# Optimization experiments

Measured on AMD Instinct MI355X. Metric: run time of the kernel, lower is better.

Reference implementation:

```python
import jax, jax.numpy as jnp
import numpy as np

EMBED = 768
NH = 12          # num_heads
NL = 3           # num_levels
NP = 4           # num_points
DV = 384         # value dim = embed_dim * deform_ratio(0.5)
DH = DV // NH    # per-head value dim = 32
B = 16
LQ = 1024        # (512/16)^2 ViT tokens
SHAPES = [(64, 64), (32, 32), (16, 16)]  # 1/8, 1/16, 1/32 pyramid of 512x512
LKV = sum(h * w for h, w in SHAPES)      # 5376
EPS = 1e-6


def layer_norm(x, w, b):
    mu = jnp.mean(x, axis=-1, keepdims=True)
    var = jnp.mean((x - mu) ** 2, axis=-1, keepdims=True)
    return (x - mu) / jnp.sqrt(var + EPS) * w + b


def bilinear_sample(v, loc, H, W):
    # v: (B, NH, H*W, DH); loc: (B, Lq, NH, P, 2) normalized in [0,1]
    # Matches torch grid_sample(align_corners=False, padding_mode='zeros').
    Bv, Lq = loc.shape[0], loc.shape[1]
    x = loc[..., 0] * W - 0.5
    y = loc[..., 1] * H - 0.5
    x0 = jnp.floor(x)
    y0 = jnp.floor(y)
    dx = x - x0
    dy = y - y0
    x0i = x0.astype(jnp.int32)
    y0i = y0.astype(jnp.int32)

    def gather(xi, yi):
        valid = (xi >= 0) & (xi < W) & (yi >= 0) & (yi < H)  # (B,Lq,NH,P)
        xc = jnp.clip(xi, 0, W - 1)
        yc = jnp.clip(yi, 0, H - 1)
        lin = (yc * W + xc).transpose(0, 2, 1, 3).reshape(Bv, NH, Lq * NP)
        g = jnp.take_along_axis(v, lin[..., None], axis=2)  # (B,NH,Lq*P,DH)
        g = g.reshape(Bv, NH, Lq, NP, DH).transpose(0, 2, 1, 3, 4)  # (B,Lq,NH,P,DH)
        return g * valid[..., None].astype(g.dtype)

    g00 = gather(x0i, y0i)
    g01 = gather(x0i + 1, y0i)
    g10 = gather(x0i, y0i + 1)
    g11 = gather(x0i + 1, y0i + 1)
    w00 = ((1 - dx) * (1 - dy))[..., None]
    w01 = (dx * (1 - dy))[..., None]
    w10 = ((1 - dx) * dy)[..., None]
    w11 = (dx * dy)[..., None]
    return g00 * w00 + g01 * w01 + g10 * w10 + g11 * w11


def ms_deform_attn_core(value, shapes_list, loc, aw):
    # value: (B,LKV,NH,DH); loc: (B,Lq,NH,NL,NP,2); aw: (B,Lq,NH,NL,NP)
    Bv, Lq = loc.shape[0], loc.shape[1]
    samples = []
    idx = 0
    for l, (H, W) in enumerate(shapes_list):
        v = value[:, idx:idx + H * W].transpose(0, 2, 1, 3)  # (B,NH,HW,DH)
        idx += H * W
        samples.append(bilinear_sample(v, loc[:, :, :, l], H, W))
    s = jnp.stack(samples, axis=3)  # (B,Lq,NH,NL,NP,DH)
    o = jnp.einsum('bqhlp,bqhlpd->bqhd', aw, s)
    return o.reshape(Bv, Lq, NH * DH)


def setup_inputs() -> dict:
    key = jax.random.key(0)
    ks = jax.random.split(key, 12)

    def n(k, shape, s=0.02):
        return jax.random.normal(k, shape, jnp.float32) * s

    return {
        'q': jax.random.normal(ks[0], (B, LQ, EMBED), jnp.float32),
        'reference_points': jax.random.uniform(ks[1], (B, LQ, NL, 2), jnp.float32),
        'kv': jax.random.normal(ks[2], (B, LKV, EMBED), jnp.float32),
        'spatial_shapes': jnp.asarray(SHAPES, jnp.int32),
        'level_start_index': jnp.asarray(
            np.cumsum([0] + [h * w for h, w in SHAPES])[:-1], jnp.int32),
        'ln1_w': jnp.ones(EMBED, jnp.float32),
        'ln1_b': jnp.zeros(EMBED, jnp.float32),
        'ln2_w': jnp.ones(EMBED, jnp.float32),
        'ln2_b': jnp.zeros(EMBED, jnp.float32),
        'gamma': n(ks[3], (EMBED,), 0.1),
        'w_off': n(ks[4], (EMBED, NH * NL * NP * 2)),
        'b_off': n(ks[5], (NH * NL * NP * 2,), 0.01),
        'w_aw': n(ks[6], (EMBED, NH * NL * NP)),
        'b_aw': jnp.zeros(NH * NL * NP, jnp.float32),
        'w_val': n(ks[7], (EMBED, DV)),
        'b_val': jnp.zeros(DV, jnp.float32),
        'w_out': n(ks[8], (DV, EMBED)),
        'b_out': jnp.zeros(EMBED, jnp.float32),
    }


def reference(q, reference_points, kv, spatial_shapes, level_start_index,
              ln1_w, ln1_b, ln2_w, ln2_b, gamma,
              w_off, b_off, w_aw, b_aw, w_val, b_val, w_out, b_out):
    shapes_list = [tuple(int(v) for v in r) for r in np.asarray(spatial_shapes)]
    Bq, Lq, _ = q.shape
    qn = layer_norm(q, ln1_w, ln1_b)
    kvn = layer_norm(kv, ln2_w, ln2_b)
    value = (kvn @ w_val + b_val).reshape(Bq, -1, NH, DH)
    off = (qn @ w_off + b_off).reshape(Bq, Lq, NH, NL, NP, 2)
    aw = (qn @ w_aw + b_aw).reshape(Bq, Lq, NH, NL * NP)
    aw = jax.nn.softmax(aw, axis=-1).reshape(Bq, Lq, NH, NL, NP)
    # offset normalizer is (W_l, H_l) per level
    wh = jnp.asarray([[w, h] for (h, w) in shapes_list], q.dtype)  # (NL,2)
    loc = reference_points[:, :, None, :, None, :] + off / wh[None, None, None, :, None, :]
    attn = ms_deform_attn_core(value, shapes_list, loc, aw)
    attn = attn @ w_out + b_out
    return q + gamma * attn
```

## Files before the change

kernel.cpp:

```cpp
#include <hip/hip_runtime.h>

#define DEV __device__ __forceinline__

typedef short bf16x8 __attribute__((ext_vector_type(8)));
typedef float f32x4 __attribute__((ext_vector_type(4)));
typedef unsigned int u32;
typedef __attribute__((address_space(1))) const u32* gas_ptr;
typedef __attribute__((address_space(3))) u32* las_ptr;

DEV short f2bf(float f) {
  union { float f; unsigned u; } un; un.f = f;
  unsigned r = un.u + 0x7FFFu + ((un.u >> 16) & 1u);
  return (short)(r >> 16);
}
DEV float bf2f(unsigned short s) {
  union { unsigned u; float f; } un;
  un.u = ((unsigned)s) << 16;
  return un.f;
}
DEV void gload16(const short* g, short* l) {
  __builtin_amdgcn_global_load_lds((gas_ptr)g, (las_ptr)l, 16, 0, 0);
}
DEV float hsum4(float4 v) { return v.x + v.y + v.z + v.w; }

DEV void ln_row4(const float* __restrict__ x, const float* __restrict__ w,
                 const float* __restrict__ b, short* __restrict__ y,
                 const int rb) {
  const int wv = threadIdx.x >> 6, lane = threadIdx.x & 63;
  const int row = rb * 4 + wv;
  const float* xr = x + (size_t)row * 768;
  float4 v0 = *(const float4*)(xr + lane * 4);
  float4 v1 = *(const float4*)(xr + 256 + lane * 4);
  float4 v2 = *(const float4*)(xr + 512 + lane * 4);
  float s = hsum4(v0) + hsum4(v1) + hsum4(v2);
  #pragma unroll
  for (int off = 32; off > 0; off >>= 1) s += __shfl_xor(s, off, 64);
  const float mu = s * (1.f / 768.f);
  float4 d0 = make_float4(v0.x - mu, v0.y - mu, v0.z - mu, v0.w - mu);
  float4 d1 = make_float4(v1.x - mu, v1.y - mu, v1.z - mu, v1.w - mu);
  float4 d2 = make_float4(v2.x - mu, v2.y - mu, v2.z - mu, v2.w - mu);
  float vs = d0.x * d0.x + d0.y * d0.y + d0.z * d0.z + d0.w * d0.w +
             d1.x * d1.x + d1.y * d1.y + d1.z * d1.z + d1.w * d1.w +
             d2.x * d2.x + d2.y * d2.y + d2.z * d2.z + d2.w * d2.w;
  #pragma unroll
  for (int off = 32; off > 0; off >>= 1) vs += __shfl_xor(vs, off, 64);
  const float rs = rsqrtf(vs * (1.f / 768.f) + 1e-6f);
  const float4 w0 = *(const float4*)(w + lane * 4);
  const float4 w1 = *(const float4*)(w + 256 + lane * 4);
  const float4 w2 = *(const float4*)(w + 512 + lane * 4);
  const float4 b0 = *(const float4*)(b + lane * 4);
  const float4 b1 = *(const float4*)(b + 256 + lane * 4);
  const float4 b2 = *(const float4*)(b + 512 + lane * 4);
  unsigned short* yr = (unsigned short*)y + (size_t)row * 768;
  ushort4 o;
  o.x = (unsigned short)f2bf(d0.x * rs * w0.x + b0.x);
  o.y = (unsigned short)f2bf(d0.y * rs * w0.y + b0.y);
  o.z = (unsigned short)f2bf(d0.z * rs * w0.z + b0.z);
  o.w = (unsigned short)f2bf(d0.w * rs * w0.w + b0.w);
  *(ushort4*)(yr + lane * 4) = o;
  o.x = (unsigned short)f2bf(d1.x * rs * w1.x + b1.x);
  o.y = (unsigned short)f2bf(d1.y * rs * w1.y + b1.y);
  o.z = (unsigned short)f2bf(d1.z * rs * w1.z + b1.z);
  o.w = (unsigned short)f2bf(d1.w * rs * w1.w + b1.w);
  *(ushort4*)(yr + 256 + lane * 4) = o;
  o.x = (unsigned short)f2bf(d2.x * rs * w2.x + b2.x);
  o.y = (unsigned short)f2bf(d2.y * rs * w2.y + b2.y);
  o.z = (unsigned short)f2bf(d2.z * rs * w2.z + b2.z);
  o.w = (unsigned short)f2bf(d2.w * rs * w2.w + b2.w);
  *(ushort4*)(yr + 512 + lane * 4) = o;
}

__global__ __launch_bounds__(256) void fused_pre_kernel(
    const float* __restrict__ kv, const float* __restrict__ q,
    const float* __restrict__ ln2w, const float* __restrict__ ln2b,
    const float* __restrict__ ln1w, const float* __restrict__ ln1b,
    short* __restrict__ kvn, short* __restrict__ qn,
    const float* __restrict__ w_val, const float* __restrict__ w_off,
    const float* __restrict__ w_aw, const float* __restrict__ w_out,
    const float* __restrict__ b_off, const float* __restrict__ b_aw,
    short* __restrict__ wT_val, short* __restrict__ wT_offaw,
    short* __restrict__ wT_out, float* __restrict__ bias_cat) {
  const int bid = blockIdx.x;
  if (bid < 21504) { ln_row4(kv, ln2w, ln2b, kvn, bid); return; }
  if (bid < 25600) { ln_row4(q, ln1w, ln1b, qn, bid - 21504); return; }
  int g = (bid - 25600) * 256 + threadIdx.x;
  bf16x8 v;
  if (g < 36864) {
    int n = g / 96, k0 = (g % 96) * 8;
    #pragma unroll
    for (int i = 0; i < 8; i++) v[i] = f2bf(w_val[(size_t)(k0 + i) * 384 + n]);
    *(bf16x8*)&wT_val[n * 768 + k0] = v;
    return;
  }
  g -= 36864;
  if (g < 27648) {
    int n = g / 96, k0 = (g % 96) * 8;
    #pragma unroll
    for (int i = 0; i < 8; i++) v[i] = f2bf(w_off[(size_t)(k0 + i) * 288 + n]);
    *(bf16x8*)&wT_offaw[n * 768 + k0] = v;
    return;
  }
  g -= 27648;
  if (g < 13824) {
    int n = g / 96, k0 = (g % 96) * 8;
    #pragma unroll
    for (int i = 0; i < 8; i++) v[i] = f2bf(w_aw[(size_t)(k0 + i) * 144 + n]);
    *(bf16x8*)&wT_offaw[(288 + n) * 768 + k0] = v;
    return;
  }
  g -= 13824;
  if (g < 7680) {
    int n = 432 + g / 96, k0 = (g % 96) * 8;
    #pragma unroll
    for (int i = 0; i < 8; i++) v[i] = 0;
    *(bf16x8*)&wT_offaw[n * 768 + k0] = v;
    return;
  }
  g -= 7680;
  if (g < 36864) {
    int n = g / 48, k0 = (g % 48) * 8;
    #pragma unroll
    for (int i = 0; i < 8; i++) v[i] = f2bf(w_out[(size_t)(k0 + i) * 768 + n]);
    *(bf16x8*)&wT_out[n * 384 + k0] = v;
    return;
  }
  g -= 36864;
  if (g < 512) { bias_cat[g] = (g < 288) ? b_off[g] : (g < 432 ? b_aw[g - 288] : 0.f); }
}

DEV void gemm_core(const short* __restrict__ A, const short* __restrict__ Wt,
                   const int K, const int row0, const int n0,
                   short* As, short* Bs, f32x4 acc[4][4]) {
  const int tid = threadIdx.x;
  const int wave = tid >> 6, lane = tid & 63;
  const int lr = lane & 15, quad = lane >> 4;
  const int wm = wave >> 1, wn = wave & 1;

  const short* gA[2]; const short* gB[2];
  int loA[2];
  #pragma unroll
  for (int rnd = 0; rnd < 2; rnd++) {
    int G = rnd * 256 + wave * 64 + lane;
    int line = G >> 3, pos = G & 7, x = pos ^ (line & 7);
    int r = line * 2 + (x >> 2), qk = (x & 3) * 8;
    gA[rnd] = A + (size_t)(row0 + r) * K + qk;
    gB[rnd] = Wt + (size_t)(n0 + r) * K + qk;
    loA[rnd] = (rnd * 256 + wave * 64) * 8;
  }

  int aOff[4], bOff[4];
  #pragma unroll
  for (int t4 = 0; t4 < 4; t4++) {
    int r = wm * 64 + t4 * 16 + lr;
    int pos = ((r & 1) * 4 + quad) ^ ((r >> 1) & 7);
    aOff[t4] = ((r >> 1) * 8 + pos) * 8;
    int rb = wn * 64 + t4 * 16 + lr;
    int posb = ((rb & 1) * 4 + quad) ^ ((rb >> 1) & 7);
    bOff[t4] = ((rb >> 1) * 8 + posb) * 8;
  }

  #pragma unroll
  for (int i = 0; i < 4; i++)
    #pragma unroll
    for (int j = 0; j < 4; j++)
      #pragma unroll
      for (int e = 0; e < 4; e++) acc[i][j][e] = 0.f;

  const int nt = K >> 5;
  gload16(gA[0], As + loA[0]);
  gload16(gA[1], As + loA[1]);
  gload16(gB[0], Bs + loA[0]);
  gload16(gB[1], Bs + loA[1]);
  gA[0] += 32; gA[1] += 32; gB[0] += 32; gB[1] += 32;

  int cur = 0;
  for (int t = 0; t < nt; ++t) {
    if (t + 1 < nt) {
      const int nb = (cur ^ 1) * 4096;
      gload16(gA[0], As + nb + loA[0]);
      gload16(gA[1], As + nb + loA[1]);
      gload16(gB[0], Bs + nb + loA[0]);
      gload16(gB[1], Bs + nb + loA[1]);
      gA[0] += 32; gA[1] += 32; gB[0] += 32; gB[1] += 32;
      asm volatile("s_waitcnt vmcnt(4)" ::: "memory");
    } else {
      asm volatile("s_waitcnt vmcnt(0)" ::: "memory");
    }
    asm volatile("s_barrier" ::: "memory");
    const int cb = cur * 4096;
    bf16x8 av[4], bv[4];
    #pragma unroll
    for (int t4 = 0; t4 < 4; t4++) {
      av[t4] = *(const bf16x8*)(As + cb + aOff[t4]);
      bv[t4] = *(const bf16x8*)(Bs + cb + bOff[t4]);
    }
    #pragma unroll
    for (int ct = 0; ct < 4; ct++)
      #pragma unroll
      for (int rt = 0; rt < 4; rt++)
        acc[rt][ct] = __builtin_amdgcn_mfma_f32_16x16x32_bf16(av[rt], bv[ct], acc[rt][ct], 0, 0, 0);
    asm volatile("s_barrier" ::: "memory");
    cur ^= 1;
  }
}

__global__ __launch_bounds__(256, 3) void gemm_dual_kernel(
    const short* __restrict__ A0, const short* __restrict__ W0,
    const float* __restrict__ b0, short* __restrict__ C0,
    const short* __restrict__ A1, const short* __restrict__ W1,
    const float* __restrict__ b1, float* __restrict__ C1) {
  __shared__ __align__(16) short As[2 * 128 * 32];
  __shared__ __align__(16) short Bs[2 * 128 * 32];
  const int id = blockIdx.x;
  const int swz = (id & 7) * 316 + (id >> 3);
  const bool isval = swz < 2016;
  const short* A; const short* Wt; const float* bias;
  int row0, n0, N;
  if (isval) {
    A = A0; Wt = W0; bias = b0; N = 384;
    n0 = (swz % 3) * 128; row0 = (swz / 3) * 128;
  } else {
    const int o = swz - 2016;
    A = A1; Wt = W1; bias = b1; N = 512;
    n0 = (o & 3) * 128; row0 = (o >> 2) * 128;
  }
  f32x4 acc[4][4];
  gemm_core(A, Wt, 768, row0, n0, As, Bs, acc);

  const int lane = threadIdx.x & 63, wave = threadIdx.x >> 6;
  const int lr = lane & 15, quad = lane >> 4;
  const int wm = wave >> 1, wn = wave & 1;
  #pragma unroll
  for (int ct = 0; ct < 4; ct++) {
    const int n = n0 + wn * 64 + ct * 16 + lr;
    const float bs = bias[n];
    #pragma unroll
    for (int rt = 0; rt < 4; rt++) {
      #pragma unroll
      for (int i = 0; i < 4; i++) {
        const int m = row0 + wm * 64 + rt * 16 + quad * 4 + i;
        const float v = acc[rt][ct][i] + bs;
        if (isval) C0[(size_t)m * 384 + n] = f2bf(v);
        else       C1[(size_t)m * 512 + n] = v;
      }
    }
  }
}

__global__ __launch_bounds__(256, 3) void gemm_final_kernel(
    const short* __restrict__ A, const short* __restrict__ Wt,
    const float* __restrict__ bias, const float* __restrict__ qres,
    const float* __restrict__ gamma, float* __restrict__ Cout) {
  __shared__ __align__(16) short As[2 * 128 * 32];
  __shared__ __align__(16) short Bs[2 * 128 * 32];
  const int id = blockIdx.x;
  const int swz = (id & 7) * 96 + (id >> 3);
  const int n0 = (swz % 6) * 128, row0 = (swz / 6) * 128;
  f32x4 acc[4][4];
  gemm_core(A, Wt, 384, row0, n0, As, Bs, acc);

  const int lane = threadIdx.x & 63, wave = threadIdx.x >> 6;
  const int lr = lane & 15, quad = lane >> 4;
  const int wm = wave >> 1, wn = wave & 1;
  #pragma unroll
  for (int ct = 0; ct < 4; ct++) {
    const int n = n0 + wn * 64 + ct * 16 + lr;
    const float bs = bias[n];
    const float gm = gamma[n];
    #pragma unroll
    for (int rt = 0; rt < 4; rt++) {
      #pragma unroll
      for (int i = 0; i < 4; i++) {
        const int m = row0 + wm * 64 + rt * 16 + quad * 4 + i;
        Cout[(size_t)m * 768 + n] =
            qres[(size_t)m * 768 + n] + gm * (acc[rt][ct][i] + bs);
      }
    }
  }
}

__global__ __launch_bounds__(384) void sampler_kernel(
    const float* __restrict__ offaw,
    const float* __restrict__ refp,
    const short* __restrict__ value,
    short* __restrict__ o) {
  const int tid = threadIdx.x;
  const int qi = tid / 96, t = tid % 96;
  const int head = t >> 3, ln4 = t & 7;
  const int blk = (blockIdx.x & 7) * 512 + (blockIdx.x >> 3);
  const int bq = blk * 4 + qi;
  __shared__ __align__(16) float s[4][440];
  __shared__ float sref[4][6];
  const float* row = offaw + (size_t)bq * 512;
  #pragma unroll
  for (int i = t; i < 108; i += 96)
    *(float4*)&s[qi][i * 4] = *(const float4*)&row[i * 4];
  if (t < 6) sref[qi][t] = refp[(size_t)bq * 6 + t];
  __syncthreads();

  const float* awp = &s[qi][288 + head * 12];
  float mx = awp[0];
  #pragma unroll
  for (int j = 1; j < 12; j++) mx = fmaxf(mx, awp[j]);
  float wgt[12];
  float ssum = 0.f;
  #pragma unroll
  for (int j = 0; j < 12; j++) { float e = __expf(awp[j] - mx); wgt[j] = e; ssum += e; }
  const float inv = 1.f / ssum;

  const int b = bq >> 10;
  const unsigned short* vb =
      (const unsigned short*)value + (size_t)b * 5376 * 384 + head * 32 + ln4 * 4;
  float4 acc = make_float4(0.f, 0.f, 0.f, 0.f);
  const int HW[3] = {64, 32, 16};
  const int starts[3] = {0, 4096, 5120};
  #pragma unroll
  for (int l = 0; l < 3; l++) {
    const int Wi = HW[l];
    const float Wf = (float)Wi;
    const float rx = sref[qi][l * 2], ry = sref[qi][l * 2 + 1];
    const unsigned short* base = vb + (size_t)starts[l] * 384;
    #pragma unroll
    for (int p = 0; p < 4; p++) {
      const int oi = ((head * 3 + l) * 4 + p) * 2;
      float x = fmaf(rx, Wf, s[qi][oi] - 0.5f);
      float y = fmaf(ry, Wf, s[qi][oi + 1] - 0.5f);
      float xf = floorf(x), yf = floorf(y);
      float dx = x - xf, dy = y - yf;
      int x0 = (int)xf, y0 = (int)yf;
      int x1 = x0 + 1, y1 = y0 + 1;
      int x0c = min(max(x0, 0), Wi - 1), x1c = min(max(x1, 0), Wi - 1);
      int y0c = min(max(y0, 0), Wi - 1), y1c = min(max(y1, 0), Wi - 1);
      float wx0 = (x0 >= 0 && x0 < Wi) ? (1.f - dx) : 0.f;
      float wx1 = (x1 < Wi && x1 >= 0) ? dx : 0.f;
      float wy0 = (y0 >= 0 && y0 < Wi) ? (1.f - dy) : 0.f;
      float wy1 = (y1 < Wi && y1 >= 0) ? dy : 0.f;
      const ushort4 u00 = *(const ushort4*)(base + (size_t)(y0c * Wi + x0c) * 384);
      const ushort4 u01 = *(const ushort4*)(base + (size_t)(y0c * Wi + x1c) * 384);
      const ushort4 u10 = *(const ushort4*)(base + (size_t)(y1c * Wi + x0c) * 384);
      const ushort4 u11 = *(const ushort4*)(base + (size_t)(y1c * Wi + x1c) * 384);
      const float w00 = wx0 * wy0, w01 = wx1 * wy0, w10 = wx0 * wy1, w11 = wx1 * wy1;
      const float g = wgt[l * 4 + p];
      acc.x += g * (w00 * bf2f(u00.x) + w01 * bf2f(u01.x) + w10 * bf2f(u10.x) + w11 * bf2f(u11.x));
      acc.y += g * (w00 * bf2f(u00.y) + w01 * bf2f(u01.y) + w10 * bf2f(u10.y) + w11 * bf2f(u11.y));
      acc.z += g * (w00 * bf2f(u00.z) + w01 * bf2f(u01.z) + w10 * bf2f(u10.z) + w11 * bf2f(u11.z));
      acc.w += g * (w00 * bf2f(u00.w) + w01 * bf2f(u01.w) + w10 * bf2f(u10.w) + w11 * bf2f(u11.w));
    }
  }
  ushort4 outv;
  outv.x = (unsigned short)f2bf(acc.x * inv);
  outv.y = (unsigned short)f2bf(acc.y * inv);
  outv.z = (unsigned short)f2bf(acc.z * inv);
  outv.w = (unsigned short)f2bf(acc.w * inv);
  *(ushort4*)((unsigned short*)o + (size_t)bq * 384 + head * 32 + ln4 * 4) = outv;
}

extern "C" void kernel_launch(void* const* d_in, const int* in_sizes, int n_in,
                              void* d_out, int out_size, void* d_ws, size_t ws_size,
                              hipStream_t stream) {
  (void)in_sizes; (void)n_in; (void)out_size; (void)ws_size;
  const float* q     = (const float*)d_in[0];
  const float* refp  = (const float*)d_in[1];
  const float* kv    = (const float*)d_in[2];
  const float* ln1w  = (const float*)d_in[5];
  const float* ln1b  = (const float*)d_in[6];
  const float* ln2w  = (const float*)d_in[7];
  const float* ln2b  = (const float*)d_in[8];
  const float* gamma = (const float*)d_in[9];
  const float* w_off = (const float*)d_in[10];
  const float* b_off = (const float*)d_in[11];
  const float* w_aw  = (const float*)d_in[12];
  const float* b_aw  = (const float*)d_in[13];
  const float* w_val = (const float*)d_in[14];
  const float* b_val = (const float*)d_in[15];
  const float* w_out = (const float*)d_in[16];
  const float* b_out = (const float*)d_in[17];
  float* out = (float*)d_out;

  char* wsp = (char*)d_ws;
  size_t cur = 0;
  auto alloc = [&](size_t bytes) -> void* {
    cur = (cur + 255) & ~(size_t)255;
    void* p = wsp + cur;
    cur += bytes;
    return p;
  };
  short*  wT_val   = (short*)alloc((size_t)384 * 768 * 2);
  short*  wT_offaw = (short*)alloc((size_t)512 * 768 * 2);
  short*  wT_out   = (short*)alloc((size_t)768 * 384 * 2);
  float*  bias_cat = (float*)alloc((size_t)512 * 4);
  short*  kvn      = (short*)alloc((size_t)86016 * 768 * 2);
  short*  qn       = (short*)alloc((size_t)16384 * 768 * 2);
  short*  value    = (short*)alloc((size_t)86016 * 384 * 2);
  float*  offaw    = (float*)alloc((size_t)16384 * 512 * 4);
  short*  obuf     = (short*)alloc((size_t)16384 * 384 * 2);

  fused_pre_kernel<<<26082, 256, 0, stream>>>(
      kv, q, ln2w, ln2b, ln1w, ln1b, kvn, qn,
      w_val, w_off, w_aw, w_out, b_off, b_aw,
      wT_val, wT_offaw, wT_out, bias_cat);
  gemm_dual_kernel<<<2528, 256, 0, stream>>>(
      kvn, wT_val, b_val, value, qn, wT_offaw, bias_cat, offaw);
  sampler_kernel<<<4096, 384, 0, stream>>>(offaw, refp, value, obuf);
  gemm_final_kernel<<<768, 256, 0, stream>>>(
      obuf, wT_out, b_out, q, gamma, out);
}
```

Baseline: 655.2 us.

## Triple-buffer GEMM LDS pipeline and precompute sampler indices and weights in shared memory

The GEMM core moves from double to triple buffering, prefetching two K-tiles ahead with adjusted vmcnt waits and an explicit lgkmcnt drain before the barrier. This is meant to hide more global-load latency, at the cost of 50% more LDS per block, which may reduce occupancy. The sampler now computes the softmax and the bilinear corner indices and weights once per (query, head, level, point) in shared memory, instead of repeating them in each of the 8 lanes per head. The gather loop then only reads these precomputed values, removing redundant ALU work.

```diff
diff --git a/kernel.cpp b/kernel.cpp
--- a/kernel.cpp
+++ b/kernel.cpp
@@ -167,21 +167,27 @@
       for (int e = 0; e < 4; e++) acc[i][j][e] = 0.f;
 
   const int nt = K >> 5;
-  gload16(gA[0], As + loA[0]);
-  gload16(gA[1], As + loA[1]);
-  gload16(gB[0], Bs + loA[0]);
-  gload16(gB[1], Bs + loA[1]);
-  gA[0] += 32; gA[1] += 32; gB[0] += 32; gB[1] += 32;
+  #pragma unroll
+  for (int pb = 0; pb < 2; pb++) {
+    const int bb = pb * 4096;
+    gload16(gA[0], As + bb + loA[0]);
+    gload16(gA[1], As + bb + loA[1]);
+    gload16(gB[0], Bs + bb + loA[0]);
+    gload16(gB[1], Bs + bb + loA[1]);
+    gA[0] += 32; gA[1] += 32; gB[0] += 32; gB[1] += 32;
+  }
 
   int cur = 0;
   for (int t = 0; t < nt; ++t) {
-    if (t + 1 < nt) {
-      const int nb = (cur ^ 1) * 4096;
+    if (t + 2 < nt) {
+      const int nb = (cur == 0 ? 2 : cur - 1) * 4096;
       gload16(gA[0], As + nb + loA[0]);
       gload16(gA[1], As + nb + loA[1]);
       gload16(gB[0], Bs + nb + loA[0]);
       gload16(gB[1], Bs + nb + loA[1]);
       gA[0] += 32; gA[1] += 32; gB[0] += 32; gB[1] += 32;
+      asm volatile("s_waitcnt vmcnt(8)" ::: "memory");
+    } else if (t + 1 < nt) {
       asm volatile("s_waitcnt vmcnt(4)" ::: "memory");
     } else {
       asm volatile("s_waitcnt vmcnt(0)" ::: "memory");
@@ -199,8 +205,10 @@
       #pragma unroll
       for (int rt = 0; rt < 4; rt++)
         acc[rt][ct] = __builtin_amdgcn_mfma_f32_16x16x32_bf16(av[rt], bv[ct], acc[rt][ct], 0, 0, 0);
+    asm volatile("s_waitcnt lgkmcnt(0)" ::: "memory");
+    __builtin_amdgcn_sched_barrier(0);
     asm volatile("s_barrier" ::: "memory");
-    cur ^= 1;
+    cur = (cur == 2) ? 0 : cur + 1;
   }
 }
 
@@ -209,19 +217,19 @@
     const float* __restrict__ b0, short* __restrict__ C0,
     const short* __restrict__ A1, const short* __restrict__ W1,
     const float* __restrict__ b1, float* __restrict__ C1) {
-  __shared__ __align__(16) short As[2 * 128 * 32];
-  __shared__ __align__(16) short Bs[2 * 128 * 32];
+  __shared__ __align__(16) short As[3 * 128 * 32];
+  __shared__ __align__(16) short Bs[3 * 128 * 32];
   const int id = blockIdx.x;
   const int swz = (id & 7) * 316 + (id >> 3);
   const bool isval = swz < 2016;
   const short* A; const short* Wt; const float* bias;
-  int row0, n0, N;
+  int row0, n0;
   if (isval) {
-    A = A0; Wt = W0; bias = b0; N = 384;
+    A = A0; Wt = W0; bias = b0;
     n0 = (swz % 3) * 128; row0 = (swz / 3) * 128;
   } else {
     const int o = swz - 2016;
-    A = A1; Wt = W1; bias = b1; N = 512;
+    A = A1; Wt = W1; bias = b1;
     n0 = (o & 3) * 128; row0 = (o >> 2) * 128;
   }
   f32x4 acc[4][4];
@@ -251,8 +259,8 @@
     const short* __restrict__ A, const short* __restrict__ Wt,
     const float* __restrict__ bias, const float* __restrict__ qres,
     const float* __restrict__ gamma, float* __restrict__ Cout) {
-  __shared__ __align__(16) short As[2 * 128 * 32];
-  __shared__ __align__(16) short Bs[2 * 128 * 32];
+  __shared__ __align__(16) short As[3 * 128 * 32];
+  __shared__ __align__(16) short Bs[3 * 128 * 32];
   const int id = blockIdx.x;
   const int swz = (id & 7) * 96 + (id >> 3);
   const int n0 = (swz % 6) * 128, row0 = (swz / 6) * 128;
@@ -285,73 +293,97 @@
     const short* __restrict__ value,
     short* __restrict__ o) {
   const int tid = threadIdx.x;
+  const int blk = (blockIdx.x & 7) * 512 + (blockIdx.x >> 3);
+  const int bq0 = blk * 4;
+  __shared__ __align__(16) float s[4][440];
+  __shared__ float sref[4][6];
+  __shared__ float snw[48][12];
+  __shared__ __align__(8) ushort4 slin[576];
+  __shared__ __align__(16) float4 sw[576];
+
+  {
+    const int qi = tid / 96, t = tid % 96;
+    const float* row = offaw + (size_t)(bq0 + qi) * 512;
+    #pragma unroll
+    for (int i = t; i < 108; i += 96)
+      *(float4*)&s[qi][i * 4] = *(const float4*)&row[i * 4];
+    if (t < 6) sref[qi][t] = refp[(size_t)(bq0 + qi) * 6 + t];
+  }
+  __syncthreads();
+
+  if (tid < 48) {
+    const int qi = tid / 12, h = tid % 12;
+    const float* awp = &s[qi][288 + h * 12];
+    float mx = awp[0];
+    #pragma unroll
+    for (int j = 1; j < 12; j++) mx = fmaxf(mx, awp[j]);
+    float e[12], ssum = 0.f;
+    #pragma unroll
+    for (int j = 0; j < 12; j++) { e[j] = __expf(awp[j] - mx); ssum += e[j]; }
+    const float inv = 1.f / ssum;
+    #pragma unroll
+    for (int j = 0; j < 12; j++) snw[tid][j] = e[j] * inv;
+  }
+  for (int tu = tid; tu < 576; tu += 384) {
+    const int qi = tu / 144, rem = tu % 144;
+    const int h = rem / 12, lp = rem % 12, l = lp >> 2, p = lp & 3;
+    const int Wi = 64 >> l;
+    const float Wf = (float)Wi;
+    const float rx = sref[qi][l * 2], ry = sref[qi][l * 2 + 1];
+    const int oi = ((h * 3 + l) * 4 + p) * 2;
+    float x = fmaf(rx, Wf, s[qi][oi] - 0.5f);
+    float y = fmaf(ry, Wf, s[qi][oi + 1] - 0.5f);
+    float xf = floorf(x), yf = floorf(y);
+    float dx = x - xf, dy = y - yf;
+    int x0 = (int)xf, y0 = (int)yf;
+    int x1 = x0 + 1, y1 = y0 + 1;
+    int x0c = min(max(x0, 0), Wi - 1), x1c = min(max(x1, 0), Wi - 1);
+    int y0c = min(max(y0, 0), Wi - 1), y1c = min(max(y1, 0), Wi - 1);
+    float wx0 = (x0 >= 0 && x0 < Wi) ? (1.f - dx) : 0.f;
+    float wx1 = (x1 < Wi && x1 >= 0) ? dx : 0.f;
+    float wy0 = (y0 >= 0 && y0 < Wi) ? (1.f - dy) : 0.f;
+    float wy1 = (y1 < Wi && y1 >= 0) ? dy : 0.f;
+    const int st = (l == 0) ? 0 : (l == 1 ? 4096 : 5120);
+    ushort4 lv;
+    lv.x = (unsigned short)(st + y0c * Wi + x0c);
+    lv.y = (unsigned short)(st + y0c * Wi + x1c);
+    lv.z = (unsigned short)(st + y1c * Wi + x0c);
+    lv.w = (unsigned short)(st + y1c * Wi + x1c);
+    slin[tu] = lv;
+    sw[tu] = make_float4(wx0 * wy0, wx1 * wy0, wx0 * wy1, wx1 * wy1);
+  }
+  __syncthreads();
+
   const int qi = tid / 96, t = tid % 96;
   const int head = t >> 3, ln4 = t & 7;
-  const int blk = (blockIdx.x & 7) * 512 + (blockIdx.x >> 3);
-  const int bq = blk * 4 + qi;
-  __shared__ __align__(16) float s[4][440];
-  __shared__ float sref[4][6];
-  const float* row = offaw + (size_t)bq * 512;
-  #pragma unroll
-  for (int i = t; i < 108; i += 96)
-    *(float4*)&s[qi][i * 4] = *(const float4*)&row[i * 4];
-  if (t < 6) sref[qi][t] = refp[(size_t)bq * 6 + t];
-  __syncthreads();
-
-  const float* awp = &s[qi][288 + head * 12];
-  float mx = awp[0];
-  #pragma unroll
-  for (int j = 1; j < 12; j++) mx = fmaxf(mx, awp[j]);
-  float wgt[12];
-  float ssum = 0.f;
-  #pragma unroll
-  for (int j = 0; j < 12; j++) { float e = __expf(awp[j] - mx); wgt[j] = e; ssum += e; }
-  const float inv = 1.f / ssum;
-
+  const int bq = bq0 + qi;
   const int b = bq >> 10;
   const unsigned short* vb =
       (const unsigned short*)value + (size_t)b * 5376 * 384 + head * 32 + ln4 * 4;
   float4 acc = make_float4(0.f, 0.f, 0.f, 0.f);
-  const int HW[3] = {64, 32, 16};
-  const int starts[3] = {0, 4096, 5120};
-  #pragma unroll
-  for (int l = 0; l < 3; l++) {
-    const int Wi = HW[l];
-    const float Wf = (float)Wi;
-    const float rx = sref[qi][l * 2], ry = sref[qi][l * 2 + 1];
-    const unsigned short* base = vb + (size_t)starts[l] * 384;
-    #pragma unroll
-    for (int p = 0; p < 4; p++) {
-      const int oi = ((head * 3 + l) * 4 + p) * 2;
-      float x = fmaf(rx, Wf, s[qi][oi] - 0.5f);
-      float y = fmaf(ry, Wf, s[qi][oi + 1] - 0.5f);
-      float xf = floorf(x), yf = floorf(y);
-      float dx = x - xf, dy = y - yf;
-      int x0 = (int)xf, y0 = (int)yf;
-      int x1 = x0 + 1, y1 = y0 + 1;
-      int x0c = min(max(x0, 0), Wi - 1), x1c = min(max(x1, 0), Wi - 1);
-      int y0c = min(max(y0, 0), Wi - 1), y1c = min(max(y1, 0), Wi - 1);
-      float wx0 = (x0 >= 0 && x0 < Wi) ? (1.f - dx) : 0.f;
-      float wx1 = (x1 < Wi && x1 >= 0) ? dx : 0.f;
-      float wy0 = (y0 >= 0 && y0 < Wi) ? (1.f - dy) : 0.f;
-      float wy1 = (y1 < Wi && y1 >= 0) ? dy : 0.f;
-      const ushort4 u00 = *(const ushort4*)(base + (size_t)(y0c * Wi + x0c) * 384);
-      const ushort4 u01 = *(const ushort4*)(base + (size_t)(y0c * Wi + x1c) * 384);
-      const ushort4 u10 = *(const ushort4*)(base + (size_t)(y1c * Wi + x0c) * 384);
-      const ushort4 u11 = *(const ushort4*)(base + (size_t)(y1c * Wi + x1c) * 384);
-      const float w00 = wx0 * wy0, w01 = wx1 * wy0, w10 = wx0 * wy1, w11 = wx1 * wy1;
-      const float g = wgt[l * 4 + p];
-      acc.x += g * (w00 * bf2f(u00.x) + w01 * bf2f(u01.x) + w10 * bf2f(u10.x) + w11 * bf2f(u11.x));
-      acc.y += g * (w00 * bf2f(u00.y) + w01 * bf2f(u01.y) + w10 * bf2f(u10.y) + w11 * bf2f(u11.y));
-      acc.z += g * (w00 * bf2f(u00.z) + w01 * bf2f(u01.z) + w10 * bf2f(u10.z) + w11 * bf2f(u11.z));
-      acc.w += g * (w00 * bf2f(u00.w) + w01 * bf2f(u01.w) + w10 * bf2f(u10.w) + w11 * bf2f(u11.w));
-    }
+  const int tub = qi * 144 + head * 12;
+  const float* nwp = snw[qi * 12 + head];
+  #pragma unroll
+  for (int lp = 0; lp < 12; lp++) {
+    const int tu = tub + lp;
+    const float g = nwp[lp];
+    const ushort4 lv = slin[tu];
+    const float4 wv = sw[tu];
+    const ushort4 u00 = *(const ushort4*)(vb + (size_t)lv.x * 384);
+    const ushort4 u01 = *(const ushort4*)(vb + (size_t)lv.y * 384);
+    const ushort4 u10 = *(const ushort4*)(vb + (size_t)lv.z * 384);
+    const ushort4 u11 = *(const ushort4*)(vb + (size_t)lv.w * 384);
+    const float w00 = g * wv.x, w01 = g * wv.y, w10 = g * wv.z, w11 = g * wv.w;
+    acc.x += w00 * bf2f(u00.x) + w01 * bf2f(u01.x) + w10 * bf2f(u10.x) + w11 * bf2f(u11.x);
+    acc.y += w00 * bf2f(u00.y) + w01 * bf2f(u01.y) + w10 * bf2f(u10.y) + w11 * bf2f(u11.y);
+    acc.z += w00 * bf2f(u00.z) + w01 * bf2f(u01.z) + w10 * bf2f(u10.z) + w11 * bf2f(u11.z);
+    acc.w += w00 * bf2f(u00.w) + w01 * bf2f(u01.w) + w10 * bf2f(u10.w) + w11 * bf2f(u11.w);
   }
   ushort4 outv;
-  outv.x = (unsigned short)f2bf(acc.x * inv);
-  outv.y = (unsigned short)f2bf(acc.y * inv);
-  outv.z = (unsigned short)f2bf(acc.z * inv);
-  outv.w = (unsigned short)f2bf(acc.w * inv);
+  outv.x = (unsigned short)f2bf(acc.x);
+  outv.y = (unsigned short)f2bf(acc.y);
+  outv.z = (unsigned short)f2bf(acc.z);
+  outv.w = (unsigned short)f2bf(acc.w);
   *(ushort4*)((unsigned short*)o + (size_t)bq * 384 + head * 32 + ln4 * 4) = outv;
 }
 
```

Measured after the change: 640.9 us. -2.2%, faster.
